# Performance work log

Hardware: AMD Instinct MI355X
Metric: run time of the kernel (lower is better)

The kernel has to match this reference:

```python
import jax, jax.numpy as jnp
import numpy as np

TEMPERATURE = 0.05
SCALE = 0.02  # keeps distances/T small enough that exp(-d/T) does not underflow


def setup_inputs() -> dict:
    key = jax.random.key(0)
    k1, k2 = jax.random.split(key)
    B, D = 4096, 1024
    text_embeddings = jax.random.normal(k1, (B, D), dtype=jnp.float32) * SCALE
    image_embeddings = jax.random.normal(k2, (B, D), dtype=jnp.float32) * SCALE
    return {"text_embeddings": text_embeddings, "image_embeddings": image_embeddings}


def reference(text_embeddings, image_embeddings):
    B = text_embeddings.shape[0]
    # Pairwise L2 distances between every image_i and every text_j without
    # materializing a [B, B, D] diff tensor: ||a||^2 + ||b||^2 - 2 a.b
    img_sq = jnp.sum(image_embeddings * image_embeddings, axis=1)   # [B]
    txt_sq = jnp.sum(text_embeddings * text_embeddings, axis=1)     # [B]
    cross = jnp.einsum('id,jd->ij', image_embeddings, text_embeddings)  # [B, B]
    sq_dist = img_sq[:, None] + txt_sq[None, :] - 2.0 * cross
    dist = jnp.sqrt(jnp.maximum(sq_dist, 0.0))                      # [B, B]
    sim = jnp.exp(-dist / TEMPERATURE)                              # [B, B]
    numerator = jnp.diagonal(sim)                                   # sim[i, i]
    denominator = jnp.sum(sim, axis=1) - numerator                  # off-diagonal row sum
    per_sample = jnp.where(denominator != 0.0,
                           -jnp.log(numerator / denominator),
                           0.0)
    return jnp.sum(per_sample) / B
```

## Files before the change

kernel.cpp:

```cpp
#include <hip/hip_runtime.h>
#include <hip/hip_bf16.h>
#include <math.h>

#define BSZ 4096
#define DSZ 1024
#define BM  256
#define BN  256
#define BK  64
#define NT  16
#define NIT 8

typedef unsigned short u16;
typedef __attribute__((ext_vector_type(8))) short bf16x8;
typedef __attribute__((ext_vector_type(4))) float f32x4;

__device__ inline u16 f2bf_rne(float f) {
    unsigned int u = __float_as_uint(f);
    u += 0x7fffu + ((u >> 16) & 1u);
    return (u16)(u >> 16);
}

__global__ __launch_bounds__(256) void cvt_norm_kernel(
        const float* __restrict__ img, const float* __restrict__ txt,
        u16* __restrict__ imgb, u16* __restrict__ txtb,
        float* __restrict__ img_sq, float* __restrict__ txt_sq,
        float* __restrict__ rowsum) {
    const int row = blockIdx.x;
    const bool isTxt = (blockIdx.y != 0);
    const float* __restrict__ src = isTxt ? txt : img;
    u16* __restrict__ dst = isTxt ? txtb : imgb;
    float* __restrict__ sq = isTxt ? txt_sq : img_sq;

    const int t = threadIdx.x;
    const float4 v = reinterpret_cast<const float4*>(src + (size_t)row * DSZ)[t];

    ushort4 o;
    o.x = f2bf_rne(v.x); o.y = f2bf_rne(v.y);
    o.z = f2bf_rne(v.z); o.w = f2bf_rne(v.w);
    reinterpret_cast<ushort4*>(dst + (size_t)row * DSZ)[t] = o;

    float s = v.x * v.x + v.y * v.y + v.z * v.z + v.w * v.w;
    #pragma unroll
    for (int off = 32; off; off >>= 1) s += __shfl_down(s, off);

    __shared__ float lds[4];
    if ((t & 63) == 0) lds[t >> 6] = s;
    __syncthreads();
    if (t == 0) {
        sq[row] = lds[0] + lds[1] + lds[2] + lds[3];
        if (!isTxt) rowsum[row] = 0.0f;
    }
}

__global__ __launch_bounds__(512, 2) void fused_mfma_kernel(
        const u16* __restrict__ imgb, const u16* __restrict__ txtb,
        const float* __restrict__ img_sq, const float* __restrict__ txt_sq,
        float* __restrict__ rowsum, float* __restrict__ diag_dist) {

    extern __shared__ char smem[];

    const int lin = blockIdx.y * 16 + blockIdx.x;
    const int sw  = (lin & 7) * 32 + (lin >> 3);
    const int bi = sw >> 4, bj = sw & 15;

    const int tid  = threadIdx.x;
    const int lane = tid & 63;
    const int w    = tid >> 6;
    const int wr   = w >> 2;
    const int wc   = w & 3;
    const int lr   = lane >> 4;
    const int lc   = lane & 15;
    const int swz  = lc & 7;

    const int ib0 = bi * BM;
    const int jb0 = bj * BN;

    auto stageHT = [&](int mat, int kt, int h) {
        const u16* base   = mat ? txtb : imgb;
        const int rowbase = mat ? jb0 : ib0;
        const int xoff    = mat ? 65536 : 0;
        const int b = kt & 1;
        #pragma unroll
        for (int j = 0; j < 2; ++j) {
            const int row_h = j * 64 + (tid >> 3);
            const int gch   = (tid & 7) ^ (row_h & 7);
            const u16* g = base + (size_t)(rowbase + h * 128 + row_h) * DSZ
                                + kt * BK + gch * 8;
            char* dst = smem + xoff + b * 32768 + h * 16384 + j * 8192 + w * 1024;
            __builtin_amdgcn_global_load_lds(
                (const __attribute__((address_space(1))) void*)g,
                (__attribute__((address_space(3))) void*)dst, 16, 0, 0);
        }
    };

    stageHT(0, 0, 0); stageHT(0, 0, 1);
    stageHT(1, 0, 0); stageHT(1, 0, 1);
    stageHT(1, 1, 0); stageHT(1, 1, 1);
    asm volatile("s_waitcnt vmcnt(4)" ::: "memory");
    __builtin_amdgcn_s_barrier();

    f32x4 acc[8][4] = {};
    bf16x8 bfr[2][4];

    const char* Ab[2] = { smem + wr * 16384,
                          smem + 32768 + wr * 16384 };
    const char* Bb[2] = { smem + 65536 + (wc >> 1) * 16384,
                          smem + 65536 + 32768 + (wc >> 1) * 16384 };
    const int rboff = (wc & 1) * 64;

    for (int i = 0; i < NIT; ++i) {
        const bool more = (i < NIT - 1);
        #pragma unroll
        for (int p = 0; p < 8; ++p) {
            const int tsel = p >> 2;
            const int q    = p & 3;

            if (q == 0) {
                #pragma unroll
                for (int kk = 0; kk < 2; ++kk)
                    #pragma unroll
                    for (int n = 0; n < 4; ++n)
                        bfr[kk][n] = *reinterpret_cast<const bf16x8*>(
                            Bb[tsel] + (rboff + n * 16 + lc) * 128
                                     + (((kk * 4 + lr) ^ swz) * 16));
            }
            bf16x8 afr[2][2];
            #pragma unroll
            for (int dm = 0; dm < 2; ++dm)
                #pragma unroll
                for (int kk = 0; kk < 2; ++kk)
                    afr[dm][kk] = *reinterpret_cast<const bf16x8*>(
                        Ab[tsel] + ((q * 2 + dm) * 16 + lc) * 128
                                 + (((kk * 4 + lr) ^ swz) * 16));

            if (p == 0)      stageHT(0, 2 * i + 1, 0);
            else if (p == 1) stageHT(0, 2 * i + 1, 1);
            else if (p == 2) { if (more) stageHT(1, 2 * i + 2, 0); }
            else if (p == 3) { if (more) stageHT(1, 2 * i + 2, 1); }
            else if (p == 4) { if (more) stageHT(0, 2 * i + 2, 0); }
            else if (p == 5) { if (more) stageHT(0, 2 * i + 2, 1); }
            else if (p == 6) { if (more) stageHT(1, 2 * i + 3, 0); }
            else             { if (more) stageHT(1, 2 * i + 3, 1); }

            __builtin_amdgcn_s_barrier();
            asm volatile("s_waitcnt lgkmcnt(0)" ::: "memory");
            __builtin_amdgcn_sched_barrier(0);

            __builtin_amdgcn_s_setprio(1);
            #pragma unroll
            for (int dm = 0; dm < 2; ++dm)
                #pragma unroll
                for (int n = 0; n < 4; ++n)
                    #pragma unroll
                    for (int kk = 0; kk < 2; ++kk)
                        acc[q * 2 + dm][n] = __builtin_amdgcn_mfma_f32_16x16x32_bf16(
                            afr[dm][kk], bfr[kk][n], acc[q * 2 + dm][n], 0, 0, 0);
            __builtin_amdgcn_s_setprio(0);

            if (p == 3) {
                if (more) asm volatile("s_waitcnt vmcnt(4)" ::: "memory");
                else      asm volatile("s_waitcnt vmcnt(0)" ::: "memory");
            } else if (p == 7) {
                if (more) asm volatile("s_waitcnt vmcnt(4)" ::: "memory");
            }
            __builtin_amdgcn_s_barrier();
        }
    }

    const int jw = jb0 + wc * 64;
    const int iw = ib0 + wr * 128;

    float tq[4];
    #pragma unroll
    for (int n = 0; n < 4; ++n) tq[n] = txt_sq[jw + n * 16 + lc];

    float rs[8][4];
    #pragma unroll
    for (int m = 0; m < 8; ++m) {
        #pragma unroll
        for (int j = 0; j < 4; ++j) {
            const int gi = iw + m * 16 + lr * 4 + j;
            const float iq = img_sq[gi];
            float s = 0.0f;
            #pragma unroll
            for (int n = 0; n < 4; ++n) {
                const float d2 = iq + tq[n] - 2.0f * acc[m][n][j];
                const float d  = sqrtf(fmaxf(d2, 0.0f));
                const float sim = __expf(-20.0f * d);
                s += sim;
                if (gi == jw + n * 16 + lc) diag_dist[gi] = d;
            }
            rs[m][j] = s;
        }
    }

    #pragma unroll
    for (int off = 1; off < 16; off <<= 1)
        #pragma unroll
        for (int m = 0; m < 8; ++m)
            #pragma unroll
            for (int j = 0; j < 4; ++j)
                rs[m][j] += __shfl_xor(rs[m][j], off);

    if (lc == 0) {
        #pragma unroll
        for (int m = 0; m < 8; ++m)
            #pragma unroll
            for (int j = 0; j < 4; ++j)
                atomicAdd(&rowsum[iw + m * 16 + lr * 4 + j], rs[m][j]);
    }
}

__global__ __launch_bounds__(256) void finalize_kernel(
        const float* __restrict__ rowsum, const float* __restrict__ diag_dist,
        float* __restrict__ out) {
    const int tid = threadIdx.x;
    float s = 0.0f;
    for (int i = tid; i < BSZ; i += 256) {
        const float d   = diag_dist[i];
        const float num = __expf(-20.0f * d);
        const float den = rowsum[i] - num;
        s += (den != 0.0f) ? (20.0f * d + logf(den)) : 0.0f;
    }
    #pragma unroll
    for (int off = 32; off; off >>= 1) s += __shfl_down(s, off);

    __shared__ float lds[4];
    if ((tid & 63) == 0) lds[tid >> 6] = s;
    __syncthreads();
    if (tid == 0) out[0] = (lds[0] + lds[1] + lds[2] + lds[3]) * (1.0f / (float)BSZ);
}

extern "C" void kernel_launch(void* const* d_in, const int* in_sizes, int n_in,
                              void* d_out, int out_size, void* d_ws, size_t ws_size,
                              hipStream_t stream) {
    const float* txt = (const float*)d_in[0];
    const float* img = (const float*)d_in[1];
    float* out = (float*)d_out;

    u16* imgb = (u16*)d_ws;
    u16* txtb = imgb + (size_t)BSZ * DSZ;
    float* fws     = (float*)(txtb + (size_t)BSZ * DSZ);
    float* rowsum  = fws;
    float* diag    = fws + BSZ;
    float* img_sq  = fws + 2 * BSZ;
    float* txt_sq  = fws + 3 * BSZ;

    (void)hipFuncSetAttribute((const void*)fused_mfma_kernel,
                              hipFuncAttributeMaxDynamicSharedMemorySize, 131072);

    cvt_norm_kernel<<<dim3(BSZ, 2), 256, 0, stream>>>(img, txt, imgb, txtb,
                                                      img_sq, txt_sq, rowsum);

    fused_mfma_kernel<<<dim3(BSZ / BN, BSZ / BM), 512, 131072, stream>>>(
        imgb, txtb, img_sq, txt_sq, rowsum, diag);

    finalize_kernel<<<1, 256, 0, stream>>>(rowsum, diag, out);
}
```

Measured before the change: 127.8 us.

## Double-buffer LDS fragment reads and rebalance global prefetch schedule in MFMA loop

The main GEMM loop now prefetches the next phase's A and B fragments from LDS into a second register set while the current MFMAs run, and waits with partial lgkmcnt counts instead of draining all LDS reads. The global-to-LDS staging order and the vmcnt waits are reshuffled so loads issue earlier and are spread across phases. Separately, the conversion/norm kernel now handles one row per wave with four float4 loads per lane, which removes the LDS reduction and block barrier. This raises register pressure, and the hand-tuned wait counts carry correctness risk if they do not match the number of outstanding loads.

```diff
diff --git a/kernel.cpp b/kernel.cpp
--- a/kernel.cpp
+++ b/kernel.cpp
@@ -25,30 +25,30 @@
         u16* __restrict__ imgb, u16* __restrict__ txtb,
         float* __restrict__ img_sq, float* __restrict__ txt_sq,
         float* __restrict__ rowsum) {
-    const int row = blockIdx.x;
-    const bool isTxt = (blockIdx.y != 0);
-    const float* __restrict__ src = isTxt ? txt : img;
-    u16* __restrict__ dst = isTxt ? txtb : imgb;
-    float* __restrict__ sq = isTxt ? txt_sq : img_sq;
-
-    const int t = threadIdx.x;
-    const float4 v = reinterpret_cast<const float4*>(src + (size_t)row * DSZ)[t];
-
-    ushort4 o;
-    o.x = f2bf_rne(v.x); o.y = f2bf_rne(v.y);
-    o.z = f2bf_rne(v.z); o.w = f2bf_rne(v.w);
-    reinterpret_cast<ushort4*>(dst + (size_t)row * DSZ)[t] = o;
-
-    float s = v.x * v.x + v.y * v.y + v.z * v.z + v.w * v.w;
-    #pragma unroll
-    for (int off = 32; off; off >>= 1) s += __shfl_down(s, off);
-
-    __shared__ float lds[4];
-    if ((t & 63) == 0) lds[t >> 6] = s;
-    __syncthreads();
-    if (t == 0) {
-        sq[row] = lds[0] + lds[1] + lds[2] + lds[3];
-        if (!isTxt) rowsum[row] = 0.0f;
+    const int wid  = blockIdx.x * 4 + (threadIdx.x >> 6);
+    const int lane = threadIdx.x & 63;
+    const bool isTxt = (wid >= BSZ);
+    const int row = isTxt ? wid - BSZ : wid;
+
+    const float* __restrict__ src = (isTxt ? txt : img) + (size_t)row * DSZ;
+    u16* __restrict__ dst = (isTxt ? txtb : imgb) + (size_t)row * DSZ;
+
+    float s = 0.0f;
+    #pragma unroll
+    for (int c = 0; c < 4; ++c) {
+        const float4 v = *reinterpret_cast<const float4*>(src + c * 256 + lane * 4);
+        ushort4 o;
+        o.x = f2bf_rne(v.x); o.y = f2bf_rne(v.y);
+        o.z = f2bf_rne(v.z); o.w = f2bf_rne(v.w);
+        *reinterpret_cast<ushort4*>(dst + c * 256 + lane * 4) = o;
+        s += v.x * v.x + v.y * v.y + v.z * v.z + v.w * v.w;
+    }
+    #pragma unroll
+    for (int off = 32; off; off >>= 1) s += __shfl_xor(s, off);
+
+    if (lane == 0) {
+        if (isTxt) txt_sq[row] = s;
+        else { img_sq[row] = s; rowsum[row] = 0.0f; }
     }
 }
 
@@ -92,15 +92,7 @@
                 (__attribute__((address_space(3))) void*)dst, 16, 0, 0);
         }
     };
-
-    stageHT(0, 0, 0); stageHT(0, 0, 1);
-    stageHT(1, 0, 0); stageHT(1, 0, 1);
-    stageHT(1, 1, 0); stageHT(1, 1, 1);
-    asm volatile("s_waitcnt vmcnt(4)" ::: "memory");
-    __builtin_amdgcn_s_barrier();
-
-    f32x4 acc[8][4] = {};
-    bf16x8 bfr[2][4];
+    auto stageB = [&](int kt) { stageHT(1, kt, 0); stageHT(1, kt, 1); };
 
     const char* Ab[2] = { smem + wr * 16384,
                           smem + 32768 + wr * 16384 };
@@ -108,42 +100,75 @@
                           smem + 65536 + 32768 + (wc >> 1) * 16384 };
     const int rboff = (wc & 1) * 64;
 
+    stageB(0);
+    stageHT(0, 0, 0);
+    stageHT(0, 0, 1);
+    stageB(1);
+    stageHT(0, 1, 0);
+    asm volatile("s_waitcnt vmcnt(8)" ::: "memory");
+    __builtin_amdgcn_s_barrier();
+
+    f32x4 acc[8][4] = {};
+    bf16x8 bfr[2][2][4];
+    bf16x8 afr[2][2][2];
+
+    #pragma unroll
+    for (int kk = 0; kk < 2; ++kk)
+        #pragma unroll
+        for (int n = 0; n < 4; ++n)
+            bfr[0][kk][n] = *reinterpret_cast<const bf16x8*>(
+                Bb[0] + (rboff + n * 16 + lc) * 128 + (((kk * 4 + lr) ^ swz) * 16));
+    #pragma unroll
+    for (int dm = 0; dm < 2; ++dm)
+        #pragma unroll
+        for (int kk = 0; kk < 2; ++kk)
+            afr[0][dm][kk] = *reinterpret_cast<const bf16x8*>(
+                Ab[0] + ((dm) * 16 + lc) * 128 + (((kk * 4 + lr) ^ swz) * 16));
+
     for (int i = 0; i < NIT; ++i) {
         const bool more = (i < NIT - 1);
         #pragma unroll
         for (int p = 0; p < 8; ++p) {
             const int tsel = p >> 2;
             const int q    = p & 3;
-
-            if (q == 0) {
+            const int np   = (p + 1) & 7;
+            const int nq   = np & 3;
+            const int ntsel = (p < 7) ? (np >> 2) : 0;
+            const int nset  = (p + 1) & 1;
+            const bool last_phase = (!more) && (p == 7);
+
+            if (!last_phase) {
+                if (nq == 0) {
+                    #pragma unroll
+                    for (int kk = 0; kk < 2; ++kk)
+                        #pragma unroll
+                        for (int n = 0; n < 4; ++n)
+                            bfr[ntsel][kk][n] = *reinterpret_cast<const bf16x8*>(
+                                Bb[ntsel] + (rboff + n * 16 + lc) * 128
+                                          + (((kk * 4 + lr) ^ swz) * 16));
+                }
                 #pragma unroll
-                for (int kk = 0; kk < 2; ++kk)
+                for (int dm = 0; dm < 2; ++dm)
                     #pragma unroll
-                    for (int n = 0; n < 4; ++n)
-                        bfr[kk][n] = *reinterpret_cast<const bf16x8*>(
-                            Bb[tsel] + (rboff + n * 16 + lc) * 128
-                                     + (((kk * 4 + lr) ^ swz) * 16));
+                    for (int kk = 0; kk < 2; ++kk)
+                        afr[nset][dm][kk] = *reinterpret_cast<const bf16x8*>(
+                            Ab[ntsel] + ((nq * 2 + dm) * 16 + lc) * 128
+                                      + (((kk * 4 + lr) ^ swz) * 16));
             }
-            bf16x8 afr[2][2];
-            #pragma unroll
-            for (int dm = 0; dm < 2; ++dm)
-                #pragma unroll
-                for (int kk = 0; kk < 2; ++kk)
-                    afr[dm][kk] = *reinterpret_cast<const bf16x8*>(
-                        Ab[tsel] + ((q * 2 + dm) * 16 + lc) * 128
-                                 + (((kk * 4 + lr) ^ swz) * 16));
-
-            if (p == 0)      stageHT(0, 2 * i + 1, 0);
-            else if (p == 1) stageHT(0, 2 * i + 1, 1);
-            else if (p == 2) { if (more) stageHT(1, 2 * i + 2, 0); }
-            else if (p == 3) { if (more) stageHT(1, 2 * i + 2, 1); }
-            else if (p == 4) { if (more) stageHT(0, 2 * i + 2, 0); }
-            else if (p == 5) { if (more) stageHT(0, 2 * i + 2, 1); }
-            else if (p == 6) { if (more) stageHT(1, 2 * i + 3, 0); }
-            else             { if (more) stageHT(1, 2 * i + 3, 1); }
-
+
+            if (p == 0)      stageHT(0, 2 * i + 1, 1);
+            else if (p == 1) { if (more) stageB(2 * i + 2); }
+            else if (p == 2) { if (more) stageHT(0, 2 * i + 2, 0); }
+            else if (p == 4) { if (more) stageHT(0, 2 * i + 2, 1); }
+            else if (p == 5) { if (more) stageB(2 * i + 3); }
+            else if (p == 6) { if (more) stageHT(0, 2 * i + 3, 0); }
+
+            __builtin_amdgcn_sched_barrier(0);
             __builtin_amdgcn_s_barrier();
-            asm volatile("s_waitcnt lgkmcnt(0)" ::: "memory");
+
+            if (last_phase)   asm volatile("s_waitcnt lgkmcnt(0)"  ::: "memory");
+            else if (nq == 0) asm volatile("s_waitcnt lgkmcnt(12)" ::: "memory");
+            else              asm volatile("s_waitcnt lgkmcnt(4)"  ::: "memory");
             __builtin_amdgcn_sched_barrier(0);
 
             __builtin_amdgcn_s_setprio(1);
@@ -154,14 +179,17 @@
                     #pragma unroll
                     for (int kk = 0; kk < 2; ++kk)
                         acc[q * 2 + dm][n] = __builtin_amdgcn_mfma_f32_16x16x32_bf16(
-                            afr[dm][kk], bfr[kk][n], acc[q * 2 + dm][n], 0, 0, 0);
+                            afr[p & 1][dm][kk], bfr[tsel][kk][n],
+                            acc[q * 2 + dm][n], 0, 0, 0);
             __builtin_amdgcn_s_setprio(0);
 
-            if (p == 3) {
-                if (more) asm volatile("s_waitcnt vmcnt(4)" ::: "memory");
-                else      asm volatile("s_waitcnt vmcnt(0)" ::: "memory");
-            } else if (p == 7) {
-                if (more) asm volatile("s_waitcnt vmcnt(4)" ::: "memory");
+            if ((p & 1) == 0) {
+                if (more || p == 0)
+                    asm volatile("s_waitcnt vmcnt(8)" ::: "memory");
+                else if (p == 2)
+                    asm volatile("s_waitcnt vmcnt(2)" ::: "memory");
+                else
+                    asm volatile("s_waitcnt vmcnt(0)" ::: "memory");
             }
             __builtin_amdgcn_s_barrier();
         }
@@ -249,8 +277,8 @@
     (void)hipFuncSetAttribute((const void*)fused_mfma_kernel,
                               hipFuncAttributeMaxDynamicSharedMemorySize, 131072);
 
-    cvt_norm_kernel<<<dim3(BSZ, 2), 256, 0, stream>>>(img, txt, imgb, txtb,
-                                                      img_sq, txt_sq, rowsum);
+    cvt_norm_kernel<<<2048, 256, 0, stream>>>(img, txt, imgb, txtb,
+                                              img_sq, txt_sq, rowsum);
 
     fused_mfma_kernel<<<dim3(BSZ / BN, BSZ / BM), 512, 131072, stream>>>(
         imgb, txtb, img_sq, txt_sq, rowsum, diag);
```

After: 149.4 us. +16.9%, slower.

## Coalesce B-tile prefetches, drop sched barrier, and use one wave per row in convert

Applied to the files above, without the earlier changes.

The GEMM main loop now issues each full B tile prefetch in one phase instead of spreading its two halves over two phases. A prefetches are grouped the same way, and the existing vmcnt waits stay correct for the new order. The sched_barrier after the LDS wait is removed, so the compiler can interleave fragment loads with MFMAs. The bf16 convert/norm kernel now gives each wavefront one row, which removes the LDS reduction and the block-level syncthreads. The risks are burstier memory traffic and a looser instruction schedule around the MFMA block.

```diff
diff --git a/kernel.cpp b/kernel.cpp
--- a/kernel.cpp
+++ b/kernel.cpp
@@ -25,30 +25,30 @@
         u16* __restrict__ imgb, u16* __restrict__ txtb,
         float* __restrict__ img_sq, float* __restrict__ txt_sq,
         float* __restrict__ rowsum) {
-    const int row = blockIdx.x;
-    const bool isTxt = (blockIdx.y != 0);
-    const float* __restrict__ src = isTxt ? txt : img;
-    u16* __restrict__ dst = isTxt ? txtb : imgb;
-    float* __restrict__ sq = isTxt ? txt_sq : img_sq;
-
-    const int t = threadIdx.x;
-    const float4 v = reinterpret_cast<const float4*>(src + (size_t)row * DSZ)[t];
-
-    ushort4 o;
-    o.x = f2bf_rne(v.x); o.y = f2bf_rne(v.y);
-    o.z = f2bf_rne(v.z); o.w = f2bf_rne(v.w);
-    reinterpret_cast<ushort4*>(dst + (size_t)row * DSZ)[t] = o;
-
-    float s = v.x * v.x + v.y * v.y + v.z * v.z + v.w * v.w;
-    #pragma unroll
-    for (int off = 32; off; off >>= 1) s += __shfl_down(s, off);
-
-    __shared__ float lds[4];
-    if ((t & 63) == 0) lds[t >> 6] = s;
-    __syncthreads();
-    if (t == 0) {
-        sq[row] = lds[0] + lds[1] + lds[2] + lds[3];
-        if (!isTxt) rowsum[row] = 0.0f;
+    const int wid  = blockIdx.x * 4 + (threadIdx.x >> 6);
+    const int lane = threadIdx.x & 63;
+    const bool isTxt = (wid >= BSZ);
+    const int row = isTxt ? wid - BSZ : wid;
+
+    const float* __restrict__ src = (isTxt ? txt : img) + (size_t)row * DSZ;
+    u16* __restrict__ dst = (isTxt ? txtb : imgb) + (size_t)row * DSZ;
+
+    float s = 0.0f;
+    #pragma unroll
+    for (int c = 0; c < 4; ++c) {
+        const float4 v = *reinterpret_cast<const float4*>(src + c * 256 + lane * 4);
+        ushort4 o;
+        o.x = f2bf_rne(v.x); o.y = f2bf_rne(v.y);
+        o.z = f2bf_rne(v.z); o.w = f2bf_rne(v.w);
+        *reinterpret_cast<ushort4*>(dst + c * 256 + lane * 4) = o;
+        s += v.x * v.x + v.y * v.y + v.z * v.z + v.w * v.w;
+    }
+    #pragma unroll
+    for (int off = 32; off; off >>= 1) s += __shfl_xor(s, off);
+
+    if (lane == 0) {
+        if (isTxt) txt_sq[row] = s;
+        else { img_sq[row] = s; rowsum[row] = 0.0f; }
     }
 }
 
@@ -92,21 +92,23 @@
                 (__attribute__((address_space(3))) void*)dst, 16, 0, 0);
         }
     };
-
-    stageHT(0, 0, 0); stageHT(0, 0, 1);
-    stageHT(1, 0, 0); stageHT(1, 0, 1);
-    stageHT(1, 1, 0); stageHT(1, 1, 1);
-    asm volatile("s_waitcnt vmcnt(4)" ::: "memory");
-    __builtin_amdgcn_s_barrier();
-
-    f32x4 acc[8][4] = {};
-    bf16x8 bfr[2][4];
+    auto stageA = [&](int kt) { stageHT(0, kt, 0); stageHT(0, kt, 1); };
+    auto stageB = [&](int kt) { stageHT(1, kt, 0); stageHT(1, kt, 1); };
 
     const char* Ab[2] = { smem + wr * 16384,
                           smem + 32768 + wr * 16384 };
     const char* Bb[2] = { smem + 65536 + (wc >> 1) * 16384,
                           smem + 65536 + 32768 + (wc >> 1) * 16384 };
     const int rboff = (wc & 1) * 64;
+
+    stageB(0);
+    stageA(0);
+    stageB(1);
+    asm volatile("s_waitcnt vmcnt(4)" ::: "memory");
+    __builtin_amdgcn_s_barrier();
+
+    f32x4 acc[8][4] = {};
+    bf16x8 bfr[2][4];
 
     for (int i = 0; i < NIT; ++i) {
         const bool more = (i < NIT - 1);
@@ -133,18 +135,14 @@
                         Ab[tsel] + ((q * 2 + dm) * 16 + lc) * 128
                                  + (((kk * 4 + lr) ^ swz) * 16));
 
-            if (p == 0)      stageHT(0, 2 * i + 1, 0);
-            else if (p == 1) stageHT(0, 2 * i + 1, 1);
-            else if (p == 2) { if (more) stageHT(1, 2 * i + 2, 0); }
-            else if (p == 3) { if (more) stageHT(1, 2 * i + 2, 1); }
+            if (p == 0)      stageA(2 * i + 1);
+            else if (p == 1) { if (more) stageB(2 * i + 2); }
             else if (p == 4) { if (more) stageHT(0, 2 * i + 2, 0); }
             else if (p == 5) { if (more) stageHT(0, 2 * i + 2, 1); }
-            else if (p == 6) { if (more) stageHT(1, 2 * i + 3, 0); }
-            else             { if (more) stageHT(1, 2 * i + 3, 1); }
+            else if (p == 6) { if (more) stageB(2 * i + 3); }
 
             __builtin_amdgcn_s_barrier();
             asm volatile("s_waitcnt lgkmcnt(0)" ::: "memory");
-            __builtin_amdgcn_sched_barrier(0);
 
             __builtin_amdgcn_s_setprio(1);
             #pragma unroll
@@ -249,8 +247,8 @@
     (void)hipFuncSetAttribute((const void*)fused_mfma_kernel,
                               hipFuncAttributeMaxDynamicSharedMemorySize, 131072);
 
-    cvt_norm_kernel<<<dim3(BSZ, 2), 256, 0, stream>>>(img, txt, imgb, txtb,
-                                                      img_sq, txt_sq, rowsum);
+    cvt_norm_kernel<<<2048, 256, 0, stream>>>(img, txt, imgb, txtb,
+                                              img_sq, txt_sq, rowsum);
 
     fused_mfma_kernel<<<dim3(BSZ / BN, BSZ / BM), 512, 131072, stream>>>(
         imgb, txtb, img_sq, txt_sq, rowsum, diag);
```

New measurement: 127.7 us. About the same (-0.1%).
